# Performance work log

Measured on AMD Instinct MI355X. Metric: run time of the kernel, lower is better.

## Reference

```python
import jax, jax.numpy as jnp
import numpy as np

K = 32
D = 64
N_ITER = 10


def setup_inputs() -> dict:
    key = jax.random.key(0)
    k1, k2 = jax.random.split(key)
    B = 65536
    x = jax.random.normal(k1, (B, D), dtype=jnp.float32)
    c = jnp.zeros((K,), dtype=jnp.float32)
    mu = jax.random.normal(k2, (K, D), dtype=jnp.float32) * 0.1
    A = jnp.tile(jnp.eye(D, dtype=jnp.float32)[None], (K, 1, 1))
    alpha = jnp.float32(0.1)
    return {"x": x, "c": c, "mu": mu, "A": A, "alpha": alpha}


def _grad_phi(x, c, mu, A):
    # Precision matrices Sigma_i^{-1} = A_i^T A_i : (k, d, d)
    P = jnp.einsum('kji,kjl->kil', A, A)
    diff = x[:, None, :] - mu[None, :, :]          # (B, k, d)
    Pd = jnp.einsum('kij,bkj->bki', P, diff)       # Sigma^{-1} (x - mu)
    quad = jnp.einsum('bki,bki->bk', diff, Pd)     # (B, k)
    # Analytic gradient of phi(x) = logsumexp_i(c_i - 0.5 q_i):
    # grad = -sum_i softmax_i(c_i - 0.5 q_i) * Sigma_i^{-1}(x - mu_i)
    w = jax.nn.softmax(c[None, :] - 0.5 * quad, axis=1)  # (B, k)
    return -jnp.einsum('bk,bki->bi', w, Pd)


def reference(x, c, mu, A, alpha):
    def step(x_cur, _):
        x_new = x_cur + alpha * _grad_phi(x_cur, c, mu, A)
        return x_new, None
    x_final, _ = jax.lax.scan(step, x, None, length=N_ITER)
    return x_final
```

## Files before the change

### kernel.cpp

```cpp
#include <hip/hip_runtime.h>
#include <hip/hip_bf16.h>


typedef __attribute__((ext_vector_type(4))) float f32x4;
typedef __attribute__((ext_vector_type(8))) short bf16x8;

#define KC 32
#define NITER 10
#define XROW 72
#define WT_PITCH 40
#define PW_BYTES 7168

static __device__ __forceinline__ unsigned pk_bf16(float a, float b) {
  __hip_bfloat16 ha = __float2bfloat16(a), hb = __float2bfloat16(b);
  unsigned short ua = *(unsigned short*)&ha, ub = *(unsigned short*)&hb;
  return (unsigned)ua | ((unsigned)ub << 16);
}

static __device__ __forceinline__ float red16(float x) {
#if __has_builtin(__builtin_amdgcn_permlane16_swap)
  int xi = __float_as_int(x);
  auto pr = __builtin_amdgcn_permlane16_swap(xi, xi, false, false);
  return __int_as_float(pr[0]) + __int_as_float(pr[1]);
#else
  int v = __builtin_amdgcn_ds_swizzle(__float_as_int(x), 0x401F);
  return x + __int_as_float(v);
#endif
}
static __device__ __forceinline__ float red32(float x) {
  int xi = __float_as_int(x);
  auto pr = __builtin_amdgcn_permlane32_swap(xi, xi, false, false);
  return __int_as_float(pr[0]) + __int_as_float(pr[1]);
}

__global__ void precompute1(const float* __restrict__ A, const float* __restrict__ mu,
                            const float* __restrict__ c,
                            float* __restrict__ Pmu_g, float* __restrict__ e_g,
                            __hip_bfloat16* __restrict__ Psw) {
  __shared__ float As[64 * 64];
  __shared__ float Pk[64 * 64];
  const int k = blockIdx.x, tid = threadIdx.x;
  const float* Ak = A + k * 4096;
  for (int idx = tid; idx < 1024; idx += 256)
    *(f32x4*)&As[idx * 4] = *(const f32x4*)&Ak[idx * 4];
  __syncthreads();

  const int i = tid >> 2, lg = tid & 3;
  float acc[16] = {};
  for (int j = 0; j < 64; ++j) {
    float ai = As[j * 64 + i];
    const f32x4* row = (const f32x4*)&As[j * 64 + lg * 16];
#pragma unroll
    for (int g = 0; g < 4; ++g) {
      f32x4 v = row[g];
#pragma unroll
      for (int r = 0; r < 4; ++r) acc[g * 4 + r] += ai * v[r];
    }
  }
#pragma unroll
  for (int g = 0; g < 4; ++g)
#pragma unroll
    for (int r = 0; r < 4; ++r) Pk[i * 64 + lg * 16 + g * 4 + r] = acc[g * 4 + r];
  __syncthreads();

  if (tid < 64) {
    float s = 0.f;
    for (int l = 0; l < 64; ++l) s += Pk[l * 64 + tid] * mu[k * 64 + l];
    Pmu_g[k * 64 + tid] = s;
    float v = mu[k * 64 + tid] * s;
#pragma unroll
    for (int off = 1; off < 64; off <<= 1) v += __shfl_xor(v, off, 64);
    if (tid == 0) e_g[k] = c[k] - 0.5f * v;
  }

  unsigned* Psw32 = (unsigned*)(Psw + k * 4096);
  for (int idx2 = tid; idx2 < 2048; idx2 += 256) {
    int idx = idx2 << 1;
    int f = idx >> 9, ln = (idx >> 3) & 63, j = idx & 7;
    int mt = f >> 1, s = f & 1, qq = ln >> 4, l4 = ln & 15;
    int col = mt * 16 + l4, rb = s * 32 + qq * 8 + j;
    Psw32[idx2] = pk_bf16(Pk[rb * 64 + col], Pk[(rb + 1) * 64 + col]);
  }
}

__launch_bounds__(256, 2)
__global__ void denoise_main(const float* __restrict__ x_in,
                             const float* __restrict__ e_g,
                             const float* __restrict__ alpha_g,
                             const __hip_bfloat16* __restrict__ Psw,
                             const float* __restrict__ Pmu_g,
                             float* __restrict__ out) {
  __shared__ __attribute__((aligned(16))) char scratch[4 * PW_BYTES];
  __shared__ __attribute__((aligned(16))) __hip_bfloat16 pmuA_s[2048];
  __shared__ __attribute__((aligned(16))) __hip_bfloat16 pmuB_s[2048];

  const int tid = threadIdx.x;
  const int wave = tid >> 6, lane = tid & 63;
  const int q = lane >> 4, l4 = lane & 15;
  const int base_pt = blockIdx.x * 128 + wave * 32;
  const float alpha = alpha_g[0];

  char* pw = scratch + wave * PW_BYTES;
  __hip_bfloat16* xsw = (__hip_bfloat16*)pw;
  float* pmxw = (float*)pw;
  __hip_bfloat16* wtw = (__hip_bfloat16*)(pw + 4608);

  const bf16x8* PswF = (const bf16x8*)Psw;

  for (int idx = tid; idx < 2048; idx += 256) {
    int f = idx >> 9, ln = (idx >> 3) & 63, j = idx & 7;
    int mtc = f >> 1, s = f & 1, qq = ln >> 4, l4i = ln & 15;
    pmuA_s[idx] = __float2bfloat16(Pmu_g[(mtc * 16 + l4i) * 64 + s * 32 + qq * 8 + j]);
  }
  for (int idx = tid; idx < 2048; idx += 256) {
    int f = idx >> 9, ln = (idx >> 3) & 63, j = idx & 7;
    int qq = ln >> 4, l4i = ln & 15;
    pmuB_s[idx] = __float2bfloat16(Pmu_g[(qq * 8 + j) * 64 + f * 16 + l4i]);
  }

  f32x4 xm[4][2];
#pragma unroll
  for (int mt = 0; mt < 4; ++mt)
#pragma unroll
    for (int nt = 0; nt < 2; ++nt)
      xm[mt][nt] = *(const f32x4*)&x_in[(base_pt + nt * 16 + l4) * 64 + mt * 16 + q * 4];

  f32x4 ev[2];
#pragma unroll
  for (int mtc = 0; mtc < 2; ++mtc) ev[mtc] = *(const f32x4*)&e_g[mtc * 16 + q * 4];

  const f32x4 Z4 = {0.f, 0.f, 0.f, 0.f};
  const bf16x8* PmuAF = (const bf16x8*)pmuA_s;
  const bf16x8* PmuBF = (const bf16x8*)pmuB_s;

  __syncthreads();

#pragma unroll 1
  for (int it = 0; it < NITER; ++it) {
#pragma unroll
    for (int mt = 0; mt < 4; ++mt)
#pragma unroll
      for (int nt = 0; nt < 2; ++nt) {
        uint2 v;
        v.x = pk_bf16(xm[mt][nt][0], xm[mt][nt][1]);
        v.y = pk_bf16(xm[mt][nt][2], xm[mt][nt][3]);
        *(uint2*)&xsw[(nt * 16 + l4) * XROW + mt * 16 + q * 4] = v;
      }

    bf16x8 bx[2][2];
#pragma unroll
    for (int s = 0; s < 2; ++s)
#pragma unroll
      for (int nt = 0; nt < 2; ++nt)
        bx[s][nt] = *(const bf16x8*)&xsw[(nt * 16 + l4) * XROW + s * 32 + q * 8];

    bf16x8 ap[2][4][2];
#pragma unroll
    for (int mt = 0; mt < 4; ++mt)
#pragma unroll
      for (int s = 0; s < 2; ++s)
        ap[0][mt][s] = PswF[(mt * 2 + s) * 64 + lane];

    f32x4 pmx[2][2];
    __builtin_amdgcn_s_setprio(1);
#pragma unroll
    for (int mtc = 0; mtc < 2; ++mtc)
#pragma unroll
      for (int nt = 0; nt < 2; ++nt)
        pmx[mtc][nt] =
            __builtin_amdgcn_mfma_f32_16x16x32_bf16(PmuAF[(mtc * 2) * 64 + lane], bx[0][nt], Z4, 0, 0, 0);
#pragma unroll
    for (int mtc = 0; mtc < 2; ++mtc)
#pragma unroll
      for (int nt = 0; nt < 2; ++nt)
        pmx[mtc][nt] = __builtin_amdgcn_mfma_f32_16x16x32_bf16(PmuAF[(mtc * 2 + 1) * 64 + lane],
                                                               bx[1][nt], pmx[mtc][nt], 0, 0, 0);
    __builtin_amdgcn_s_setprio(0);
#pragma unroll
    for (int mtc = 0; mtc < 2; ++mtc)
#pragma unroll
      for (int nt = 0; nt < 2; ++nt)
#pragma unroll
        for (int r = 0; r < 4; ++r)
          pmxw[(mtc * 16 + q * 4 + r) * 32 + nt * 16 + l4] = pmx[mtc][nt][r] + ev[mtc][r];

    f32x4 accY[4][2];
#pragma unroll
    for (int mt = 0; mt < 4; ++mt)
#pragma unroll
      for (int nt = 0; nt < 2; ++nt) accY[mt][nt] = Z4;
    float lsum0 = 0.f, lsum1 = 0.f;

#pragma unroll 2
    for (int k = 0; k < KC; ++k) {
      const int cur = k & 1, nxt = cur ^ 1;
      const int kn = (k + 1) & (KC - 1);
#pragma unroll
      for (int mt = 0; mt < 4; ++mt)
#pragma unroll
        for (int s = 0; s < 2; ++s)
          ap[nxt][mt][s] = PswF[kn * 512 + (mt * 2 + s) * 64 + lane];

      f32x4 y[4][2];
      __builtin_amdgcn_s_setprio(1);
#pragma unroll
      for (int mt = 0; mt < 4; ++mt)
#pragma unroll
        for (int nt = 0; nt < 2; ++nt)
          y[mt][nt] = __builtin_amdgcn_mfma_f32_16x16x32_bf16(ap[cur][mt][0], bx[0][nt], Z4, 0, 0, 0);
#pragma unroll
      for (int mt = 0; mt < 4; ++mt)
#pragma unroll
        for (int nt = 0; nt < 2; ++nt)
          y[mt][nt] =
              __builtin_amdgcn_mfma_f32_16x16x32_bf16(ap[cur][mt][1], bx[1][nt], y[mt][nt], 0, 0, 0);
      __builtin_amdgcn_s_setprio(0);

      f32x4 d0 = xm[0][0] * y[0][0];
      f32x4 d1 = xm[0][1] * y[0][1];
#pragma unroll
      for (int mt = 1; mt < 4; ++mt) {
        d0 += xm[mt][0] * y[mt][0];
        d1 += xm[mt][1] * y[mt][1];
      }
      float xy0 = (d0[0] + d0[1]) + (d0[2] + d0[3]);
      float xy1 = (d1[0] + d1[1]) + (d1[2] + d1[3]);
      xy0 = red32(red16(xy0));
      xy1 = red32(red16(xy1));

      const float pk0 = pmxw[k * 32 + l4];
      const float pk1 = pmxw[k * 32 + 16 + l4];
      const float w0 = __expf(pk0 - 0.5f * xy0);
      const float w1 = __expf(pk1 - 0.5f * xy1);
      lsum0 += w0;
      lsum1 += w1;
      if (q == 0) {
        wtw[l4 * WT_PITCH + k] = __float2bfloat16(w0);
        wtw[(16 + l4) * WT_PITCH + k] = __float2bfloat16(w1);
      }
#pragma unroll
      for (int mt = 0; mt < 4; ++mt) {
        accY[mt][0] += w0 * y[mt][0];
        accY[mt][1] += w1 * y[mt][1];
      }
    }

    bf16x8 wtf[2];
#pragma unroll
    for (int nt = 0; nt < 2; ++nt)
      wtf[nt] = *(const bf16x8*)&wtw[(nt * 16 + l4) * WT_PITCH + q * 8];
    f32x4 pacc[4][2];
    __builtin_amdgcn_s_setprio(1);
#pragma unroll
    for (int mt = 0; mt < 4; ++mt) {
      bf16x8 a = PmuBF[mt * 64 + lane];
      pacc[mt][0] = __builtin_amdgcn_mfma_f32_16x16x32_bf16(a, wtf[0], Z4, 0, 0, 0);
      pacc[mt][1] = __builtin_amdgcn_mfma_f32_16x16x32_bf16(a, wtf[1], Z4, 0, 0, 0);
    }
    __builtin_amdgcn_s_setprio(0);

    const float c0 = alpha / lsum0;
    const float c1 = alpha / lsum1;
#pragma unroll
    for (int mt = 0; mt < 4; ++mt) {
      xm[mt][0] += c0 * (pacc[mt][0] - accY[mt][0]);
      xm[mt][1] += c1 * (pacc[mt][1] - accY[mt][1]);
    }
  }

#pragma unroll
  for (int mt = 0; mt < 4; ++mt)
#pragma unroll
    for (int nt = 0; nt < 2; ++nt)
      *(f32x4*)&out[(base_pt + nt * 16 + l4) * 64 + mt * 16 + q * 4] = xm[mt][nt];
}

extern "C" void kernel_launch(void* const* d_in, const int* in_sizes, int n_in,
                              void* d_out, int out_size, void* d_ws, size_t ws_size,
                              hipStream_t stream) {
  (void)in_sizes; (void)n_in; (void)out_size; (void)ws_size;
  const float* x = (const float*)d_in[0];
  const float* c = (const float*)d_in[1];
  const float* mu = (const float*)d_in[2];
  const float* A = (const float*)d_in[3];
  const float* alpha = (const float*)d_in[4];
  float* out = (float*)d_out;

  char* ws = (char*)d_ws;
  float* Pmu_g = (float*)(ws);
  float* e_g = (float*)(ws + 8192);
  __hip_bfloat16* Psw = (__hip_bfloat16*)(ws + 16640);

  precompute1<<<32, 256, 0, stream>>>(A, mu, c, Pmu_g, e_g, Psw);
  denoise_main<<<512, 256, 0, stream>>>(x, e_g, alpha, Psw, Pmu_g, out);
}
```

Measured before the change: 286.9 us.

## Split precompute across four column-strip blocks per component and drop setprio hints

```diff
diff --git a/kernel.cpp b/kernel.cpp
--- a/kernel.cpp
+++ b/kernel.cpp
@@ -34,58 +34,61 @@
 }
 
 __global__ void precompute1(const float* __restrict__ A, const float* __restrict__ mu,
-                            const float* __restrict__ c,
-                            float* __restrict__ Pmu_g, float* __restrict__ e_g,
+                            float* __restrict__ Pmu_g, float* __restrict__ ep_g,
                             __hip_bfloat16* __restrict__ Psw) {
   __shared__ float As[64 * 64];
-  __shared__ float Pk[64 * 64];
-  const int k = blockIdx.x, tid = threadIdx.x;
+  __shared__ float Ps[64 * 16];
+  __shared__ float Pmu_s[16];
+  const int k = blockIdx.x >> 2, st = blockIdx.x & 3, tid = threadIdx.x;
   const float* Ak = A + k * 4096;
   for (int idx = tid; idx < 1024; idx += 256)
     *(f32x4*)&As[idx * 4] = *(const f32x4*)&Ak[idx * 4];
   __syncthreads();
 
   const int i = tid >> 2, lg = tid & 3;
-  float acc[16] = {};
+  f32x4 acc = {0.f, 0.f, 0.f, 0.f};
   for (int j = 0; j < 64; ++j) {
     float ai = As[j * 64 + i];
-    const f32x4* row = (const f32x4*)&As[j * 64 + lg * 16];
-#pragma unroll
-    for (int g = 0; g < 4; ++g) {
-      f32x4 v = row[g];
-#pragma unroll
-      for (int r = 0; r < 4; ++r) acc[g * 4 + r] += ai * v[r];
-    }
-  }
-#pragma unroll
-  for (int g = 0; g < 4; ++g)
-#pragma unroll
-    for (int r = 0; r < 4; ++r) Pk[i * 64 + lg * 16 + g * 4 + r] = acc[g * 4 + r];
+    f32x4 v = *(const f32x4*)&As[j * 64 + st * 16 + lg * 4];
+    acc += ai * v;
+  }
+  *(f32x4*)&Ps[i * 16 + lg * 4] = acc;
   __syncthreads();
 
   if (tid < 64) {
+    const int c = tid & 15, lh = tid >> 4;
     float s = 0.f;
-    for (int l = 0; l < 64; ++l) s += Pk[l * 64 + tid] * mu[k * 64 + l];
-    Pmu_g[k * 64 + tid] = s;
-    float v = mu[k * 64 + tid] * s;
-#pragma unroll
-    for (int off = 1; off < 64; off <<= 1) v += __shfl_xor(v, off, 64);
-    if (tid == 0) e_g[k] = c[k] - 0.5f * v;
+#pragma unroll
+    for (int ll = 0; ll < 16; ++ll) s += Ps[(lh * 16 + ll) * 16 + c] * mu[k * 64 + lh * 16 + ll];
+    s += __shfl_xor(s, 16, 64);
+    s += __shfl_xor(s, 32, 64);
+    if (lh == 0) {
+      Pmu_s[c] = s;
+      Pmu_g[k * 64 + st * 16 + c] = s;
+    }
+  }
+  __syncthreads();
+  if (tid == 0) {
+    float v = 0.f;
+#pragma unroll
+    for (int c2 = 0; c2 < 16; ++c2) v += mu[k * 64 + st * 16 + c2] * Pmu_s[c2];
+    ep_g[k * 4 + st] = v;
   }
 
   unsigned* Psw32 = (unsigned*)(Psw + k * 4096);
-  for (int idx2 = tid; idx2 < 2048; idx2 += 256) {
-    int idx = idx2 << 1;
-    int f = idx >> 9, ln = (idx >> 3) & 63, j = idx & 7;
-    int mt = f >> 1, s = f & 1, qq = ln >> 4, l4 = ln & 15;
-    int col = mt * 16 + l4, rb = s * 32 + qq * 8 + j;
-    Psw32[idx2] = pk_bf16(Pk[rb * 64 + col], Pk[(rb + 1) * 64 + col]);
+  for (int idx2 = tid; idx2 < 512; idx2 += 256) {
+    int fl = idx2 << 1;
+    int s = fl >> 9, ln = (fl >> 3) & 63, j = fl & 7;
+    int qq = ln >> 4, l4 = ln & 15;
+    int rb = s * 32 + qq * 8 + j;
+    Psw32[st * 512 + idx2] = pk_bf16(Ps[rb * 16 + l4], Ps[(rb + 1) * 16 + l4]);
   }
 }
 
 __launch_bounds__(256, 2)
 __global__ void denoise_main(const float* __restrict__ x_in,
-                             const float* __restrict__ e_g,
+                             const float* __restrict__ c_g,
+                             const float* __restrict__ ep_g,
                              const float* __restrict__ alpha_g,
                              const __hip_bfloat16* __restrict__ Psw,
                              const float* __restrict__ Pmu_g,
@@ -127,7 +130,13 @@
 
   f32x4 ev[2];
 #pragma unroll
-  for (int mtc = 0; mtc < 2; ++mtc) ev[mtc] = *(const f32x4*)&e_g[mtc * 16 + q * 4];
+  for (int mtc = 0; mtc < 2; ++mtc)
+#pragma unroll
+    for (int r = 0; r < 4; ++r) {
+      const int cl = mtc * 16 + q * 4 + r;
+      const f32x4 ep = *(const f32x4*)&ep_g[cl * 4];
+      ev[mtc][r] = c_g[cl] - 0.5f * ((ep[0] + ep[1]) + (ep[2] + ep[3]));
+    }
 
   const f32x4 Z4 = {0.f, 0.f, 0.f, 0.f};
   const bf16x8* PmuAF = (const bf16x8*)pmuA_s;
@@ -162,7 +171,6 @@
         ap[0][mt][s] = PswF[(mt * 2 + s) * 64 + lane];
 
     f32x4 pmx[2][2];
-    __builtin_amdgcn_s_setprio(1);
 #pragma unroll
     for (int mtc = 0; mtc < 2; ++mtc)
 #pragma unroll
@@ -175,7 +183,6 @@
       for (int nt = 0; nt < 2; ++nt)
         pmx[mtc][nt] = __builtin_amdgcn_mfma_f32_16x16x32_bf16(PmuAF[(mtc * 2 + 1) * 64 + lane],
                                                                bx[1][nt], pmx[mtc][nt], 0, 0, 0);
-    __builtin_amdgcn_s_setprio(0);
 #pragma unroll
     for (int mtc = 0; mtc < 2; ++mtc)
 #pragma unroll
@@ -202,7 +209,6 @@
           ap[nxt][mt][s] = PswF[kn * 512 + (mt * 2 + s) * 64 + lane];
 
       f32x4 y[4][2];
-      __builtin_amdgcn_s_setprio(1);
 #pragma unroll
       for (int mt = 0; mt < 4; ++mt)
 #pragma unroll
@@ -214,7 +220,6 @@
         for (int nt = 0; nt < 2; ++nt)
           y[mt][nt] =
               __builtin_amdgcn_mfma_f32_16x16x32_bf16(ap[cur][mt][1], bx[1][nt], y[mt][nt], 0, 0, 0);
-      __builtin_amdgcn_s_setprio(0);
 
       f32x4 d0 = xm[0][0] * y[0][0];
       f32x4 d1 = xm[0][1] * y[0][1];
@@ -250,14 +255,12 @@
     for (int nt = 0; nt < 2; ++nt)
       wtf[nt] = *(const bf16x8*)&wtw[(nt * 16 + l4) * WT_PITCH + q * 8];
     f32x4 pacc[4][2];
-    __builtin_amdgcn_s_setprio(1);
 #pragma unroll
     for (int mt = 0; mt < 4; ++mt) {
       bf16x8 a = PmuBF[mt * 64 + lane];
       pacc[mt][0] = __builtin_amdgcn_mfma_f32_16x16x32_bf16(a, wtf[0], Z4, 0, 0, 0);
       pacc[mt][1] = __builtin_amdgcn_mfma_f32_16x16x32_bf16(a, wtf[1], Z4, 0, 0, 0);
     }
-    __builtin_amdgcn_s_setprio(0);
 
     const float c0 = alpha / lsum0;
     const float c1 = alpha / lsum1;
@@ -288,9 +291,9 @@
 
   char* ws = (char*)d_ws;
   float* Pmu_g = (float*)(ws);
-  float* e_g = (float*)(ws + 8192);
+  float* ep_g = (float*)(ws + 8192);
   __hip_bfloat16* Psw = (__hip_bfloat16*)(ws + 16640);
 
-  precompute1<<<32, 256, 0, stream>>>(A, mu, c, Pmu_g, e_g, Psw);
-  denoise_main<<<512, 256, 0, stream>>>(x, e_g, alpha, Psw, Pmu_g, out);
-}
+  precompute1<<<128, 256, 0, stream>>>(A, mu, Pmu_g, ep_g, Psw);
+  denoise_main<<<512, 256, 0, stream>>>(x, c, ep_g, alpha, Psw, Pmu_g, out);
+}
```

Result: faster. 278.8 us (-2.8%).
